# Kernel tuning notes

Hardware: AMD Instinct MI355X
Metric: run time of the kernel (lower is better)

Reference implementation:

```python
import jax, jax.numpy as jnp
import numpy as np

B, C, H, W = 128, 512, 14, 14
P = 512  # num_parts (codebook size)


def setup_inputs() -> dict:
    key = jax.random.key(0)
    k1, k2, k3 = jax.random.split(key, 3)
    fm = jax.random.normal(k1, (B, C, H, W), dtype=jnp.float32)
    embedding = jax.random.normal(k2, (B, C), dtype=jnp.float32)
    # self.w = torch.randn(P, C).clamp_(min=0)
    w = jnp.maximum(jax.random.normal(k3, (P, C), dtype=jnp.float32), 0.0)
    w_ep_sum = w  # clone of w at init
    w_ep_num = jnp.ones((P,), dtype=jnp.float32)
    return {"fm": fm, "embedding": embedding, "w": w,
            "w_ep_sum": w_ep_sum, "w_ep_num": w_ep_num, "epoch": 5}


def reference(fm, embedding, w, w_ep_sum, w_ep_num, epoch):
    b, c, h, wd = fm.shape
    p = w.shape[0]
    # NCHW -> [B, HW, C]
    x = jnp.transpose(fm, (0, 2, 3, 1)).reshape(b, h * wd, c)
    xf = x.reshape(b * h * wd, c)
    dist = (jnp.sum(xf * xf, axis=1, keepdims=True)
            + jnp.sum(w * w, axis=1)
            - 2.0 * (xf @ w.T))                      # [B*HW, P]
    assign = jax.nn.softmax(-dist.reshape(b, h * wd, p), axis=-1)
    # hard threshold: zero out weak assignments
    assign = jnp.where(assign < 1.0 / p, 0.0, assign)  # [B, HW, P]
    assign_sum = assign.mean(axis=1)                    # [B, P]

    if epoch > 2:  # epoch is a static Python int
        # relu(einsum('bn,nc->bnc').mean(1)) == relu((assign_sum @ w) / P)
        cvec = jax.nn.relu((assign_sum @ w) / p)        # [B, C]
        embedding_cat = jnp.concatenate([embedding, cvec], axis=-1)
    else:
        embedding_cat = jnp.concatenate([embedding, jnp.zeros_like(embedding)], axis=-1)

    # collect_weight (no-grad EMA-style accumulate).
    # einsum('bmn,bmc->bmnc').sum(1).sum(0) == einsum('bmn,bmc->nc') -- avoids
    # materializing the [B,M,N,C] tensor the torch code builds.
    update_w = jnp.einsum('bmn,bmc->nc', assign, x)     # [P, C]
    assign_mean = jnp.sum(assign, axis=(0, 1))          # [P]
    upd = assign_mean > 1.0
    new_w_ep_sum = jnp.where(upd[:, None], w_ep_sum + update_w, w_ep_sum)
    new_w_ep_num = jnp.where(upd, w_ep_num + assign_mean, w_ep_num)
    return embedding_cat, new_w_ep_sum, new_w_ep_num
```

## Files before the change

### kernel.cpp

```cpp
#include <hip/hip_runtime.h>
#include <hip/hip_bf16.h>

#define Bn   128
#define Cn   512
#define HWn  196
#define Mn   25088
#define Pn   512
#define MPAD 32768
#define SPLITK2 32
#define KCH  1024

#define OFF_XT     0u
#define OFF_AT     8388608u
#define OFF_PART   16777216u
#define OFF_XM     16777216u
#define OFF_WF     25165824u
#define OFF_WNORM  25296896u
#define OFF_RAWP   25297408u
#define OFF_MEAN   25428480u

#define OUT_CAT  0u
#define OUT_WSUM 131072u
#define OUT_WNUM 393216u

using bf16x8 = __attribute__((ext_vector_type(8))) short;
using f16x8  = __attribute__((ext_vector_type(8))) _Float16;
using f32x4  = __attribute__((ext_vector_type(4))) float;

__device__ __forceinline__ unsigned short f2b(float f) {
    union { float f; unsigned u; } x; x.f = f;
    unsigned r = x.u + 0x7fffu + ((x.u >> 16) & 1u);
    return (unsigned short)(r >> 16);
}

__global__ __launch_bounds__(64) void k_wnorm(const float* __restrict__ w,
                                              float* __restrict__ wn,
                                              _Float16* __restrict__ wf) {
    int n = blockIdx.x, l = threadIdx.x;
    const float* p = w + (size_t)n * Cn + l * 8;
    float4 a = *(const float4*)p;
    float4 b = *(const float4*)(p + 4);
    float s = a.x*a.x + a.y*a.y + a.z*a.z + a.w*a.w
            + b.x*b.x + b.y*b.y + b.z*b.z + b.w*b.w;
    alignas(16) _Float16 h[8];
    h[0]=(_Float16)a.x; h[1]=(_Float16)a.y; h[2]=(_Float16)a.z; h[3]=(_Float16)a.w;
    h[4]=(_Float16)b.x; h[5]=(_Float16)b.y; h[6]=(_Float16)b.z; h[7]=(_Float16)b.w;
    *(float4*)(wf + (size_t)(n >> 4) * 8192u + (size_t)(l >> 2) * 512
                 + (n & 15) * 32 + (l & 3) * 8) = *(const float4*)h;
    #pragma unroll
    for (int o = 32; o > 0; o >>= 1) s += __shfl_down(s, o);
    if (l == 0) wn[n] = s;
}

__global__ __launch_bounds__(512) void k_prep2(const float* __restrict__ fm,
                                               _Float16* __restrict__ xm,
                                               unsigned short* __restrict__ xt) {
    __shared__ _Float16 tile[64][200];
    int b = blockIdx.x;
    int cg = blockIdx.y * 64;
    int t = threadIdx.x;
    for (int i = t; i < 64 * 49; i += 512) {
        int cl = i / 49, h4 = i - cl * 49;
        float4 v = *(const float4*)(fm + ((size_t)(b * Cn + cg + cl) * HWn) + h4 * 4);
        tile[cl][h4*4+0] = (_Float16)v.x;
        tile[cl][h4*4+1] = (_Float16)v.y;
        tile[cl][h4*4+2] = (_Float16)v.z;
        tile[cl][h4*4+3] = (_Float16)v.w;
    }
    __syncthreads();
    for (int i = t; i < HWn * 8; i += 512) {
        int hw = i >> 3, seg = i & 7;
        alignas(16) _Float16 h[8];
        #pragma unroll
        for (int j = 0; j < 8; ++j) h[j] = tile[seg * 8 + j][hw];
        *(float4*)(xm + (size_t)(b * HWn + hw) * Cn + cg + seg * 8) = *(const float4*)h;
    }
    for (int i = t; i < 64 * 4 * 16; i += 512) {
        int cl = i >> 6, rem = i & 63;
        int q = rem >> 4, j4 = rem & 15;
        ushort4 o;
        if (j4 < 12) {
            o.x = f2b((float)tile[cl][q*49 + j4*4 + 0]);
            o.y = f2b((float)tile[cl][q*49 + j4*4 + 1]);
            o.z = f2b((float)tile[cl][q*49 + j4*4 + 2]);
            o.w = f2b((float)tile[cl][q*49 + j4*4 + 3]);
        } else if (j4 == 12) {
            o.x = f2b((float)tile[cl][q*49 + 48]);
            o.y = 0; o.z = 0; o.w = 0;
        } else {
            o.x = 0; o.y = 0; o.z = 0; o.w = 0;
        }
        int c = cg + cl;
        int T = c >> 4;
        int seg = b * 8 + q * 2 + (j4 >> 3);
        int k = (j4 & 7) * 4;
        *(ushort4*)(xt + (size_t)T * 524288u + (size_t)seg * 512 + (c & 15) * 32 + k) = o;
    }
}

__global__ __launch_bounds__(512, 2) void k_post(const _Float16* __restrict__ xm,
                                                 const _Float16* __restrict__ wf,
                                                 const float* __restrict__ wnorm,
                                                 unsigned short* __restrict__ at,
                                                 float* __restrict__ rawp) {
    __shared__ _Float16 As[113][72];
    __shared__ float red[2][64][4];
    __shared__ float colp[2][512];
    const int bid = blockIdx.x;
    const int b = bid >> 1, half = bid & 1;
    const int tid = threadIdx.x;
    const int wave = tid >> 6, lane = tid & 63;
    const int mq = wave >> 2, nq = wave & 3;
    const int rl = lane & 15, rq = lane >> 4;
    const int kb = rq * 8;
    const int m0 = b * 196 + half * 98;
    const int n0 = nq * 128;
    const int srow = tid >> 2;
    const int sk16 = (tid & 3) * 8;

    const _Float16* wtb = wf + (size_t)(nq * 8) * 8192u + rl * 32 + kb;

    f32x4 acc[4][8] = {};
    for (int c = 0; c < 8; ++c) {
        const int k0 = c * 64;
        __syncthreads();
        if (srow < 113) {
            const _Float16* src = xm + (size_t)(m0 + srow) * Cn + k0 + sk16;
            f16x8 v0 = *(const f16x8*)src;
            f16x8 v1 = *(const f16x8*)(src + 32);
            *(f16x8*)&As[srow][sk16]      = v0;
            *(f16x8*)&As[srow][32 + sk16] = v1;
        }
        __syncthreads();
        #pragma unroll
        for (int ks = 0; ks < 2; ++ks) {
            const int seg = c * 2 + ks;
            f16x8 a[4], bb[8];
            #pragma unroll
            for (int f = 0; f < 4; ++f)
                a[f] = *(const f16x8*)&As[mq * 49 + f * 16 + rl][ks * 32 + kb];
            #pragma unroll
            for (int g = 0; g < 8; ++g)
                bb[g] = *(const f16x8*)(wtb + (size_t)g * 8192u + seg * 512);
            #pragma unroll
            for (int f = 0; f < 4; ++f)
                #pragma unroll
                for (int g = 0; g < 8; ++g)
                    acc[f][g] = __builtin_amdgcn_mfma_f32_16x16x32_f16(a[f], bb[g], acc[f][g], 0, 0, 0);
        }
    }
    float wn[8];
    #pragma unroll
    for (int g = 0; g < 8; ++g) wn[g] = wnorm[n0 + g * 16 + rl];
    #pragma unroll
    for (int f = 0; f < 4; ++f)
        #pragma unroll
        for (int g = 0; g < 8; ++g)
            #pragma unroll
            for (int r = 0; r < 4; ++r)
                acc[f][g][r] = 2.0f * acc[f][g][r] - wn[g];
    float mx[4][4];
    #pragma unroll
    for (int f = 0; f < 4; ++f)
        #pragma unroll
        for (int r = 0; r < 4; ++r) {
            float m_ = acc[f][0][r];
            #pragma unroll
            for (int g = 1; g < 8; ++g) m_ = fmaxf(m_, acc[f][g][r]);
            #pragma unroll
            for (int o = 8; o >= 1; o >>= 1) m_ = fmaxf(m_, __shfl_xor(m_, o));
            mx[f][r] = m_;
        }
    if (rl == 0)
        #pragma unroll
        for (int f = 0; f < 4; ++f)
            #pragma unroll
            for (int r = 0; r < 4; ++r)
                red[mq][f * 16 + rq * 4 + r][nq] = mx[f][r];
    __syncthreads();
    float rmax[4][4];
    #pragma unroll
    for (int f = 0; f < 4; ++f)
        #pragma unroll
        for (int r = 0; r < 4; ++r) {
            float* q = red[mq][f * 16 + rq * 4 + r];
            rmax[f][r] = fmaxf(fmaxf(q[0], q[1]), fmaxf(q[2], q[3]));
        }
    float sm[4][4];
    #pragma unroll
    for (int f = 0; f < 4; ++f)
        #pragma unroll
        for (int r = 0; r < 4; ++r) {
            float s_ = 0.f;
            #pragma unroll
            for (int g = 0; g < 8; ++g) {
                float p = __expf(acc[f][g][r] - rmax[f][r]);
                acc[f][g][r] = p;
                s_ += p;
            }
            #pragma unroll
            for (int o = 8; o >= 1; o >>= 1) s_ += __shfl_xor(s_, o);
            sm[f][r] = s_;
        }
    __syncthreads();
    if (rl == 0)
        #pragma unroll
        for (int f = 0; f < 4; ++f)
            #pragma unroll
            for (int r = 0; r < 4; ++r)
                red[mq][f * 16 + rq * 4 + r][nq] = sm[f][r];
    __syncthreads();
    const float invP = 1.0f / 512.0f;
    #pragma unroll
    for (int f = 0; f < 4; ++f)
        #pragma unroll
        for (int r = 0; r < 4; ++r) {
            float* q = red[mq][f * 16 + rq * 4 + r];
            float inv = 1.0f / (q[0] + q[1] + q[2] + q[3]);
            #pragma unroll
            for (int g = 0; g < 8; ++g) {
                float a = acc[f][g][r] * inv;
                acc[f][g][r] = (a < invP) ? 0.0f : a;
            }
        }
    float cs[8] = {};
    #pragma unroll
    for (int g = 0; g < 8; ++g) {
        #pragma unroll
        for (int f = 0; f < 4; ++f)
            #pragma unroll
            for (int r = 0; r < 4; ++r)
                if (f * 16 + rq * 4 + r < 49) cs[g] += acc[f][g][r];
        cs[g] += __shfl_xor(cs[g], 16);
        cs[g] += __shfl_xor(cs[g], 32);
    }
    if (rq == 0)
        #pragma unroll
        for (int g = 0; g < 8; ++g) colp[mq][n0 + g * 16 + rl] = cs[g];
    __syncthreads();
    if (tid < 512) rawp[(size_t)bid * 512 + tid] = colp[0][tid] + colp[1][tid];
    const int mb = b * 256 + (half * 2 + mq) * 64;
    const int segbase = mb >> 5;
    #pragma unroll
    for (int f = 0; f < 4; ++f) {
        const int mloc = f * 16 + rq * 4;
        const int seg = segbase + (mloc >> 5);
        const int k = mloc & 31;
        #pragma unroll
        for (int g = 0; g < 8; ++g) {
            ushort4 o;
            o.x = (mloc + 0 < 49) ? f2b(acc[f][g][0]) : (unsigned short)0;
            o.y = (mloc + 1 < 49) ? f2b(acc[f][g][1]) : (unsigned short)0;
            o.z = (mloc + 2 < 49) ? f2b(acc[f][g][2]) : (unsigned short)0;
            o.w = (mloc + 3 < 49) ? f2b(acc[f][g][3]) : (unsigned short)0;
            const int T = nq * 8 + g;
            *(ushort4*)(at + (size_t)T * 524288u + (size_t)seg * 512 + rl * 32 + k) = o;
        }
    }
}

__global__ __launch_bounds__(256) void k_reduce(const float* __restrict__ rawp,
                                                const float* __restrict__ wnum,
                                                float* __restrict__ mean,
                                                float* __restrict__ outnum) {
    int n = blockIdx.x * 256 + threadIdx.x;
    float s = 0.f;
    for (int r = 0; r < 256; ++r) s += rawp[(size_t)r * Pn + n];
    mean[n] = s;
    outnum[n] = wnum[n] + (s > 1.0f ? s : 0.0f);
}

__global__ __launch_bounds__(256) void k_cvec(const float* __restrict__ rawp,
                                              const float* __restrict__ w,
                                              const float* __restrict__ emb,
                                              const int* __restrict__ epoch,
                                              float* __restrict__ out) {
    __shared__ float srow[512];
    int b = blockIdx.x, t = threadIdx.x;
    srow[t]       = rawp[(size_t)(2*b) * Pn + t]       + rawp[(size_t)(2*b+1) * Pn + t];
    srow[t + 256] = rawp[(size_t)(2*b) * Pn + t + 256] + rawp[(size_t)(2*b+1) * Pn + t + 256];
    __syncthreads();
    float a0 = 0.f, a1 = 0.f;
    for (int p = 0; p < Pn; ++p) {
        float ap = srow[p];
        a0 = fmaf(ap, w[(size_t)p * Cn + t], a0);
        a1 = fmaf(ap, w[(size_t)p * Cn + t + 256], a1);
    }
    const float sc = 1.0f / (196.0f * 512.0f);
    int ep = epoch[0];
    float c0 = (ep > 2) ? fmaxf(a0, 0.f) * sc : 0.f;
    float c1 = (ep > 2) ? fmaxf(a1, 0.f) * sc : 0.f;
    out[(size_t)b * 1024 + t]             = emb[(size_t)b * Cn + t];
    out[(size_t)b * 1024 + t + 256]       = emb[(size_t)b * Cn + t + 256];
    out[(size_t)b * 1024 + 512 + t]       = c0;
    out[(size_t)b * 1024 + 512 + t + 256] = c1;
}

__global__ __launch_bounds__(256) void k_upw_mfma(const unsigned short* __restrict__ at,
                                                  const unsigned short* __restrict__ xt,
                                                  float* __restrict__ part) {
    const int id = blockIdx.x;
    const int sp = id & 31;
    const int m  = id >> 5;
    const int tid = threadIdx.x;
    const int wave = tid >> 6, lane = tid & 63;
    const int wn = wave >> 1, wc = wave & 1;
    const int n0 = (m & 3) * 128;
    const int c0 = (m >> 2) * 128;
    const int rl = lane & 15, rq = lane >> 4;
    const int loff = rl * 32 + rq * 8;
    const int segbase = sp * 32;

    const unsigned short* pa[4];
    const unsigned short* pb[4];
    #pragma unroll
    for (int f = 0; f < 4; ++f) {
        const int Ta = (n0 >> 4) + wn * 4 + f;
        const int Tb = (c0 >> 4) + wc * 4 + f;
        pa[f] = at + (size_t)Ta * 524288u + (size_t)segbase * 512 + loff;
        pb[f] = xt + (size_t)Tb * 524288u + (size_t)segbase * 512 + loff;
    }

    f32x4 acc[4][4] = {};
    bf16x8 aC[4], bC[4], aN[4], bN[4];
    #pragma unroll
    for (int f = 0; f < 4; ++f) {
        aC[f] = *(const bf16x8*)(pa[f]);
        bC[f] = *(const bf16x8*)(pb[f]);
    }
    for (int ks = 0; ks < 32; ks += 2) {
        #pragma unroll
        for (int f = 0; f < 4; ++f) {
            aN[f] = *(const bf16x8*)(pa[f] + (ks + 1) * 512);
            bN[f] = *(const bf16x8*)(pb[f] + (ks + 1) * 512);
        }
        #pragma unroll
        for (int i = 0; i < 4; ++i)
            #pragma unroll
            for (int j = 0; j < 4; ++j)
                acc[i][j] = __builtin_amdgcn_mfma_f32_16x16x32_bf16(aC[i], bC[j], acc[i][j], 0, 0, 0);
        if (ks + 2 < 32) {
            #pragma unroll
            for (int f = 0; f < 4; ++f) {
                aC[f] = *(const bf16x8*)(pa[f] + (ks + 2) * 512);
                bC[f] = *(const bf16x8*)(pb[f] + (ks + 2) * 512);
            }
        }
        #pragma unroll
        for (int i = 0; i < 4; ++i)
            #pragma unroll
            for (int j = 0; j < 4; ++j)
                acc[i][j] = __builtin_amdgcn_mfma_f32_16x16x32_bf16(aN[i], bN[j], acc[i][j], 0, 0, 0);
    }
    float* o = part + (size_t)sp * (Pn * Cn);
    const int rq4 = rq * 4;
    #pragma unroll
    for (int i = 0; i < 4; ++i) {
        #pragma unroll
        for (int j = 0; j < 4; ++j) {
            int n = n0 + wn * 64 + i * 16 + rq4;
            int c = c0 + wc * 64 + j * 16 + rl;
            #pragma unroll
            for (int r = 0; r < 4; ++r)
                o[(size_t)(n + r) * Cn + c] = acc[i][j][r];
        }
    }
}

__global__ __launch_bounds__(256) void k_wep(const float* __restrict__ part,
                                             const float* __restrict__ mean,
                                             const float* __restrict__ wsum,
                                             float* __restrict__ out1) {
    int n = blockIdx.x, t = threadIdx.x;
    bool upd = mean[n] > 1.0f;
    #pragma unroll
    for (int cc = 0; cc < 2; ++cc) {
        int c = t + cc * 256;
        float s = 0.f;
        #pragma unroll
        for (int k = 0; k < SPLITK2; ++k)
            s += part[(size_t)k * (Pn * Cn) + (size_t)n * Cn + c];
        size_t idx = (size_t)n * Cn + c;
        out1[idx] = wsum[idx] + (upd ? s : 0.f);
    }
}

extern "C" void kernel_launch(void* const* d_in, const int* in_sizes, int n_in,
                              void* d_out, int out_size, void* d_ws, size_t ws_size,
                              hipStream_t stream) {
    const float* fm    = (const float*)d_in[0];
    const float* emb   = (const float*)d_in[1];
    const float* w     = (const float*)d_in[2];
    const float* wsum  = (const float*)d_in[3];
    const float* wnum  = (const float*)d_in[4];
    const int*   epoch = (const int*)d_in[5];
    float* out = (float*)d_out;
    float* wsf = (float*)d_ws;

    unsigned short* xtb   = (unsigned short*)(wsf + OFF_XT);
    unsigned short* atb   = (unsigned short*)(wsf + OFF_AT);
    float*          partb = wsf + OFF_PART;
    _Float16*       xmb   = (_Float16*)(wsf + OFF_XM);
    _Float16*       wfb   = (_Float16*)(wsf + OFF_WF);
    float*          wnormb = wsf + OFF_WNORM;
    float*          rawpb  = wsf + OFF_RAWP;
    float*          meanb  = wsf + OFF_MEAN;

    k_wnorm<<<512, 64, 0, stream>>>(w, wnormb, wfb);
    k_prep2<<<dim3(Bn, 8), 512, 0, stream>>>(fm, xmb, xtb);
    k_post<<<256, 512, 0, stream>>>(xmb, wfb, wnormb, atb, rawpb);
    k_reduce<<<2, 256, 0, stream>>>(rawpb, wnum, meanb, out + OUT_WNUM);
    k_cvec<<<Bn, 256, 0, stream>>>(rawpb, w, emb, epoch, out + OUT_CAT);
    k_upw_mfma<<<512, 256, 0, stream>>>(atb, xtb, partb);
    k_wep<<<Pn, 256, 0, stream>>>(partb, meanb, wsum, out + OUT_WSUM);
}
```

Before: 155.5 us.

## Pre-tile X into MFMA fragment layout and drop LDS staging in distance GEMM

```diff
diff --git a/kernel.cpp b/kernel.cpp
--- a/kernel.cpp
+++ b/kernel.cpp
@@ -13,11 +13,11 @@
 #define OFF_XT     0u
 #define OFF_AT     8388608u
 #define OFF_PART   16777216u
-#define OFF_XM     16777216u
+#define OFF_XMT    16777216u
 #define OFF_WF     25165824u
 #define OFF_WNORM  25296896u
 #define OFF_RAWP   25297408u
-#define OFF_MEAN   25428480u
+#define OFF_MEAN   25559552u
 
 #define OUT_CAT  0u
 #define OUT_WSUM 131072u
@@ -53,7 +53,7 @@
 }
 
 __global__ __launch_bounds__(512) void k_prep2(const float* __restrict__ fm,
-                                               _Float16* __restrict__ xm,
+                                               _Float16* __restrict__ xmt,
                                                unsigned short* __restrict__ xt) {
     __shared__ _Float16 tile[64][200];
     int b = blockIdx.x;
@@ -68,12 +68,20 @@
         tile[cl][h4*4+3] = (_Float16)v.w;
     }
     __syncthreads();
-    for (int i = t; i < HWn * 8; i += 512) {
-        int hw = i >> 3, seg = i & 7;
+    for (int i = t; i < 2048; i += 512) {
+        int q = i >> 9, rem = i & 511, j = rem >> 3, cgi = rem & 7;
         alignas(16) _Float16 h[8];
-        #pragma unroll
-        for (int j = 0; j < 8; ++j) h[j] = tile[seg * 8 + j][hw];
-        *(float4*)(xm + (size_t)(b * HWn + hw) * Cn + cg + seg * 8) = *(const float4*)h;
+        if (j < 49) {
+            #pragma unroll
+            for (int x = 0; x < 8; ++x) h[x] = tile[cgi * 8 + x][q * 49 + j];
+        } else {
+            #pragma unroll
+            for (int x = 0; x < 8; ++x) h[x] = (_Float16)0.f;
+        }
+        int Ti = b * 16 + q * 4 + (j >> 4);
+        int seg = (cg >> 5) + (cgi >> 2);
+        int inner = (j & 15) * 32 + (cgi & 3) * 8;
+        *(float4*)(xmt + (size_t)Ti * 8192u + (size_t)seg * 512 + inner) = *(const float4*)h;
     }
     for (int i = t; i < 64 * 4 * 16; i += 512) {
         int cl = i >> 6, rem = i & 63;
@@ -98,64 +106,67 @@
     }
 }
 
-__global__ __launch_bounds__(512, 2) void k_post(const _Float16* __restrict__ xm,
-                                                 const _Float16* __restrict__ wf,
-                                                 const float* __restrict__ wnorm,
-                                                 unsigned short* __restrict__ at,
-                                                 float* __restrict__ rawp) {
-    __shared__ _Float16 As[113][72];
-    __shared__ float red[2][64][4];
-    __shared__ float colp[2][512];
+__global__ __launch_bounds__(512) void k_post(const _Float16* __restrict__ xmt,
+                                              const _Float16* __restrict__ wf,
+                                              const float* __restrict__ wnorm,
+                                              unsigned short* __restrict__ at,
+                                              float* __restrict__ rawp) {
+    __shared__ float redmx[64][8];
+    __shared__ float redsm[64][8];
     const int bid = blockIdx.x;
-    const int b = bid >> 1, half = bid & 1;
+    const int b = bid >> 2, chunk = bid & 3;
     const int tid = threadIdx.x;
-    const int wave = tid >> 6, lane = tid & 63;
-    const int mq = wave >> 2, nq = wave & 3;
+    const int nq = tid >> 6, lane = tid & 63;
     const int rl = lane & 15, rq = lane >> 4;
-    const int kb = rq * 8;
-    const int m0 = b * 196 + half * 98;
-    const int n0 = nq * 128;
-    const int srow = tid >> 2;
-    const int sk16 = (tid & 3) * 8;
-
-    const _Float16* wtb = wf + (size_t)(nq * 8) * 8192u + rl * 32 + kb;
-
-    f32x4 acc[4][8] = {};
-    for (int c = 0; c < 8; ++c) {
-        const int k0 = c * 64;
-        __syncthreads();
-        if (srow < 113) {
-            const _Float16* src = xm + (size_t)(m0 + srow) * Cn + k0 + sk16;
-            f16x8 v0 = *(const f16x8*)src;
-            f16x8 v1 = *(const f16x8*)(src + 32);
-            *(f16x8*)&As[srow][sk16]      = v0;
-            *(f16x8*)&As[srow][32 + sk16] = v1;
-        }
-        __syncthreads();
-        #pragma unroll
-        for (int ks = 0; ks < 2; ++ks) {
-            const int seg = c * 2 + ks;
-            f16x8 a[4], bb[8];
-            #pragma unroll
-            for (int f = 0; f < 4; ++f)
-                a[f] = *(const f16x8*)&As[mq * 49 + f * 16 + rl][ks * 32 + kb];
-            #pragma unroll
-            for (int g = 0; g < 8; ++g)
-                bb[g] = *(const f16x8*)(wtb + (size_t)g * 8192u + seg * 512);
-            #pragma unroll
-            for (int f = 0; f < 4; ++f)
-                #pragma unroll
-                for (int g = 0; g < 8; ++g)
-                    acc[f][g] = __builtin_amdgcn_mfma_f32_16x16x32_f16(a[f], bb[g], acc[f][g], 0, 0, 0);
-        }
-    }
-    float wn[8];
-    #pragma unroll
-    for (int g = 0; g < 8; ++g) wn[g] = wnorm[n0 + g * 16 + rl];
+    const int loff = rl * 32 + rq * 8;
+    const int n0 = nq * 64;
+
+    const _Float16* pa[4];
+    const _Float16* pb[4];
+    #pragma unroll
+    for (int f = 0; f < 4; ++f) {
+        pa[f] = xmt + (size_t)(b * 16 + chunk * 4 + f) * 8192u + loff;
+        pb[f] = wf  + (size_t)(nq * 4 + f) * 8192u + loff;
+    }
+
+    f32x4 acc[4][4] = {};
+    f16x8 aC[4], bC[4], aN[4], bN[4];
+    #pragma unroll
+    for (int f = 0; f < 4; ++f) {
+        aC[f] = *(const f16x8*)(pa[f]);
+        bC[f] = *(const f16x8*)(pb[f]);
+    }
+    for (int seg = 0; seg < 16; seg += 2) {
+        #pragma unroll
+        for (int f = 0; f < 4; ++f) {
+            aN[f] = *(const f16x8*)(pa[f] + (seg + 1) * 512);
+            bN[f] = *(const f16x8*)(pb[f] + (seg + 1) * 512);
+        }
+        #pragma unroll
+        for (int i = 0; i < 4; ++i)
+            #pragma unroll
+            for (int j = 0; j < 4; ++j)
+                acc[i][j] = __builtin_amdgcn_mfma_f32_16x16x32_f16(aC[i], bC[j], acc[i][j], 0, 0, 0);
+        if (seg + 2 < 16) {
+            #pragma unroll
+            for (int f = 0; f < 4; ++f) {
+                aC[f] = *(const f16x8*)(pa[f] + (seg + 2) * 512);
+                bC[f] = *(const f16x8*)(pb[f] + (seg + 2) * 512);
+            }
+        }
+        #pragma unroll
+        for (int i = 0; i < 4; ++i)
+            #pragma unroll
+            for (int j = 0; j < 4; ++j)
+                acc[i][j] = __builtin_amdgcn_mfma_f32_16x16x32_f16(aN[i], bN[j], acc[i][j], 0, 0, 0);
+    }
+    float wn[4];
+    #pragma unroll
+    for (int g = 0; g < 4; ++g) wn[g] = wnorm[n0 + g * 16 + rl];
     #pragma unroll
     for (int f = 0; f < 4; ++f)
         #pragma unroll
-        for (int g = 0; g < 8; ++g)
+        for (int g = 0; g < 4; ++g)
             #pragma unroll
             for (int r = 0; r < 4; ++r)
                 acc[f][g][r] = 2.0f * acc[f][g][r] - wn[g];
@@ -164,9 +175,8 @@
     for (int f = 0; f < 4; ++f)
         #pragma unroll
         for (int r = 0; r < 4; ++r) {
-            float m_ = acc[f][0][r];
-            #pragma unroll
-            for (int g = 1; g < 8; ++g) m_ = fmaxf(m_, acc[f][g][r]);
+            float m_ = fmaxf(fmaxf(acc[f][0][r], acc[f][1][r]),
+                             fmaxf(acc[f][2][r], acc[f][3][r]));
             #pragma unroll
             for (int o = 8; o >= 1; o >>= 1) m_ = fmaxf(m_, __shfl_xor(m_, o));
             mx[f][r] = m_;
@@ -176,15 +186,16 @@
         for (int f = 0; f < 4; ++f)
             #pragma unroll
             for (int r = 0; r < 4; ++r)
-                red[mq][f * 16 + rq * 4 + r][nq] = mx[f][r];
+                redmx[f * 16 + rq * 4 + r][nq] = mx[f][r];
     __syncthreads();
     float rmax[4][4];
     #pragma unroll
     for (int f = 0; f < 4; ++f)
         #pragma unroll
         for (int r = 0; r < 4; ++r) {
-            float* q = red[mq][f * 16 + rq * 4 + r];
-            rmax[f][r] = fmaxf(fmaxf(q[0], q[1]), fmaxf(q[2], q[3]));
+            const float* q = redmx[f * 16 + rq * 4 + r];
+            rmax[f][r] = fmaxf(fmaxf(fmaxf(q[0], q[1]), fmaxf(q[2], q[3])),
+                               fmaxf(fmaxf(q[4], q[5]), fmaxf(q[6], q[7])));
         }
     float sm[4][4];
     #pragma unroll
@@ -193,7 +204,7 @@
         for (int r = 0; r < 4; ++r) {
             float s_ = 0.f;
             #pragma unroll
-            for (int g = 0; g < 8; ++g) {
+            for (int g = 0; g < 4; ++g) {
                 float p = __expf(acc[f][g][r] - rmax[f][r]);
                 acc[f][g][r] = p;
                 s_ += p;
@@ -202,30 +213,29 @@
             for (int o = 8; o >= 1; o >>= 1) s_ += __shfl_xor(s_, o);
             sm[f][r] = s_;
         }
-    __syncthreads();
     if (rl == 0)
         #pragma unroll
         for (int f = 0; f < 4; ++f)
             #pragma unroll
             for (int r = 0; r < 4; ++r)
-                red[mq][f * 16 + rq * 4 + r][nq] = sm[f][r];
+                redsm[f * 16 + rq * 4 + r][nq] = sm[f][r];
     __syncthreads();
     const float invP = 1.0f / 512.0f;
     #pragma unroll
     for (int f = 0; f < 4; ++f)
         #pragma unroll
         for (int r = 0; r < 4; ++r) {
-            float* q = red[mq][f * 16 + rq * 4 + r];
-            float inv = 1.0f / (q[0] + q[1] + q[2] + q[3]);
-            #pragma unroll
-            for (int g = 0; g < 8; ++g) {
+            const float* q = redsm[f * 16 + rq * 4 + r];
+            float inv = 1.0f / (q[0] + q[1] + q[2] + q[3] + q[4] + q[5] + q[6] + q[7]);
+            #pragma unroll
+            for (int g = 0; g < 4; ++g) {
                 float a = acc[f][g][r] * inv;
                 acc[f][g][r] = (a < invP) ? 0.0f : a;
             }
         }
-    float cs[8] = {};
-    #pragma unroll
-    for (int g = 0; g < 8; ++g) {
+    float cs[4] = {};
+    #pragma unroll
+    for (int g = 0; g < 4; ++g) {
         #pragma unroll
         for (int f = 0; f < 4; ++f)
             #pragma unroll
@@ -236,25 +246,23 @@
     }
     if (rq == 0)
         #pragma unroll
-        for (int g = 0; g < 8; ++g) colp[mq][n0 + g * 16 + rl] = cs[g];
-    __syncthreads();
-    if (tid < 512) rawp[(size_t)bid * 512 + tid] = colp[0][tid] + colp[1][tid];
-    const int mb = b * 256 + (half * 2 + mq) * 64;
-    const int segbase = mb >> 5;
+        for (int g = 0; g < 4; ++g)
+            rawp[(size_t)bid * 512 + n0 + g * 16 + rl] = cs[g];
+    const int segb = b * 8 + chunk * 2;
     #pragma unroll
     for (int f = 0; f < 4; ++f) {
         const int mloc = f * 16 + rq * 4;
-        const int seg = segbase + (mloc >> 5);
+        const int sa = segb + (mloc >> 5);
         const int k = mloc & 31;
         #pragma unroll
-        for (int g = 0; g < 8; ++g) {
+        for (int g = 0; g < 4; ++g) {
             ushort4 o;
             o.x = (mloc + 0 < 49) ? f2b(acc[f][g][0]) : (unsigned short)0;
             o.y = (mloc + 1 < 49) ? f2b(acc[f][g][1]) : (unsigned short)0;
             o.z = (mloc + 2 < 49) ? f2b(acc[f][g][2]) : (unsigned short)0;
             o.w = (mloc + 3 < 49) ? f2b(acc[f][g][3]) : (unsigned short)0;
-            const int T = nq * 8 + g;
-            *(ushort4*)(at + (size_t)T * 524288u + (size_t)seg * 512 + rl * 32 + k) = o;
+            const int T = nq * 4 + g;
+            *(ushort4*)(at + (size_t)T * 524288u + (size_t)sa * 512 + rl * 32 + k) = o;
         }
     }
 }
@@ -265,7 +273,7 @@
                                                 float* __restrict__ outnum) {
     int n = blockIdx.x * 256 + threadIdx.x;
     float s = 0.f;
-    for (int r = 0; r < 256; ++r) s += rawp[(size_t)r * Pn + n];
+    for (int r = 0; r < 512; ++r) s += rawp[(size_t)r * Pn + n];
     mean[n] = s;
     outnum[n] = wnum[n] + (s > 1.0f ? s : 0.0f);
 }
@@ -277,8 +285,14 @@
                                               float* __restrict__ out) {
     __shared__ float srow[512];
     int b = blockIdx.x, t = threadIdx.x;
-    srow[t]       = rawp[(size_t)(2*b) * Pn + t]       + rawp[(size_t)(2*b+1) * Pn + t];
-    srow[t + 256] = rawp[(size_t)(2*b) * Pn + t + 256] + rawp[(size_t)(2*b+1) * Pn + t + 256];
+    float s0 = 0.f, s1 = 0.f;
+    #pragma unroll
+    for (int q = 0; q < 4; ++q) {
+        s0 += rawp[(size_t)(4 * b + q) * Pn + t];
+        s1 += rawp[(size_t)(4 * b + q) * Pn + t + 256];
+    }
+    srow[t] = s0;
+    srow[t + 256] = s1;
     __syncthreads();
     float a0 = 0.f, a1 = 0.f;
     for (int p = 0; p < Pn; ++p) {
@@ -400,15 +414,15 @@
     unsigned short* xtb   = (unsigned short*)(wsf + OFF_XT);
     unsigned short* atb   = (unsigned short*)(wsf + OFF_AT);
     float*          partb = wsf + OFF_PART;
-    _Float16*       xmb   = (_Float16*)(wsf + OFF_XM);
+    _Float16*       xmtb  = (_Float16*)(wsf + OFF_XMT);
     _Float16*       wfb   = (_Float16*)(wsf + OFF_WF);
     float*          wnormb = wsf + OFF_WNORM;
     float*          rawpb  = wsf + OFF_RAWP;
     float*          meanb  = wsf + OFF_MEAN;
 
     k_wnorm<<<512, 64, 0, stream>>>(w, wnormb, wfb);
-    k_prep2<<<dim3(Bn, 8), 512, 0, stream>>>(fm, xmb, xtb);
-    k_post<<<256, 512, 0, stream>>>(xmb, wfb, wnormb, atb, rawpb);
+    k_prep2<<<dim3(Bn, 8), 512, 0, stream>>>(fm, xmtb, xtb);
+    k_post<<<512, 512, 0, stream>>>(xmtb, wfb, wnormb, atb, rawpb);
     k_reduce<<<2, 256, 0, stream>>>(rawpb, wnum, meanb, out + OUT_WNUM);
     k_cvec<<<Bn, 256, 0, stream>>>(rawpb, w, emb, epoch, out + OUT_CAT);
     k_upw_mfma<<<512, 256, 0, stream>>>(atb, xtb, partb);
```

After: 183.5 us. +18.0%, slower.
